# Performance work log

Measured on AMD Instinct MI355X. Metric: run time of the kernel, lower is better.

## Reference

```python
import jax, jax.numpy as jnp
import numpy as np

B, T, C, H = 2, 2048, 2048, 16
HD = C // H  # 128 head dim
ROPE_BASE = 10000.0


def setup_inputs() -> dict:
    key = jax.random.key(0)
    k0, k1, k2 = jax.random.split(key, 3)
    x = jax.random.normal(k0, (B, T, C), dtype=jnp.float32)
    W_attn = jax.random.normal(k1, (C, 3 * C), dtype=jnp.float32) * 0.02
    b_attn = jnp.zeros((3 * C,), dtype=jnp.float32)
    W_proj = jax.random.normal(k2, (C, C), dtype=jnp.float32) * 0.02
    b_proj = jnp.zeros((C,), dtype=jnp.float32)
    # freqs_cis = exp(i * t * theta_j), represented as (cos, sin), shape [T, HD//2]
    inv_freq = 1.0 / (ROPE_BASE ** (jnp.arange(0, HD, 2, dtype=jnp.float32) / HD))
    freqs = jnp.outer(jnp.arange(T, dtype=jnp.float32), inv_freq)
    return {"x": x, "W_attn": W_attn, "b_attn": b_attn, "W_proj": W_proj,
            "b_proj": b_proj, "cos": jnp.cos(freqs), "sin": jnp.sin(freqs)}


def _apply_rope(v, cos, sin):
    # v: [B, T, H, HD]; pairs (v[..., 2i], v[..., 2i+1]) rotated by angle freqs[t, i]
    vr = v.reshape(v.shape[:-1] + (-1, 2))
    x0, x1 = vr[..., 0], vr[..., 1]
    c = cos[None, :, None, :]  # [1, T, 1, HD//2]
    s = sin[None, :, None, :]
    o0 = x0 * c - x1 * s
    o1 = x0 * s + x1 * c
    return jnp.stack([o0, o1], axis=-1).reshape(v.shape)


def reference(x, W_attn, b_attn, W_proj, b_proj, cos, sin):
    Bv, Tv, Cv = x.shape
    qkv = x @ W_attn + b_attn                      # [B, T, 3C]
    q, k, v = jnp.split(qkv, 3, axis=-1)
    q = q.reshape(Bv, Tv, H, HD)
    k = k.reshape(Bv, Tv, H, HD)
    v = v.reshape(Bv, Tv, H, HD)
    q = _apply_rope(q, cos, sin)
    k = _apply_rope(k, cos, sin)
    scale = 1.0 / jnp.sqrt(jnp.float32(HD))
    att = jnp.einsum('bqhd,bkhd->bhqk', q, k) * scale
    causal = jnp.tril(jnp.ones((Tv, Tv), dtype=bool))
    att = jnp.where(causal[None, None], att, jnp.finfo(att.dtype).min)
    att = jax.nn.softmax(att, axis=-1)
    y = jnp.einsum('bhqk,bkhd->bqhd', att, v).reshape(Bv, Tv, Cv)
    return y @ W_proj + b_proj
```

## Files before the change

kernel.cpp:

```cpp
#include <hip/hip_runtime.h>

typedef unsigned short u16;
typedef __attribute__((ext_vector_type(8))) short short8;
typedef __attribute__((ext_vector_type(4))) float f32x4;

#define TSEQ 2048
#define NHEAD 16
#define HDIM 128

__device__ __forceinline__ u16 f2bf(float x) {
    unsigned u = __float_as_uint(x);
    return (u16)((u + 0x7fffu + ((u >> 16) & 1u)) >> 16);
}
__device__ __forceinline__ float b2f(u16 h) {
    return __uint_as_float(((unsigned)h) << 16);
}
__device__ __forceinline__ void async16(const void* g, void* l) {
    __builtin_amdgcn_global_load_lds((__attribute__((address_space(1))) void*)(void*)g,
                                     (__attribute__((address_space(3))) void*)l, 16, 0, 0);
}
__device__ __forceinline__ f32x4 zero4() {
    f32x4 z = {0.f, 0.f, 0.f, 0.f};
    return z;
}

template <int CTRL>
__device__ __forceinline__ float dppf(float x) {
    return __int_as_float(__builtin_amdgcn_mov_dpp(__float_as_int(x), CTRL, 0xf, 0xf, true));
}
__device__ __forceinline__ float dpp_max16(float x) {
    x = fmaxf(x, dppf<0xB1>(x));
    x = fmaxf(x, dppf<0x4E>(x));
    x = fmaxf(x, dppf<0x141>(x));
    x = fmaxf(x, dppf<0x140>(x));
    return x;
}
__device__ __forceinline__ float dpp_sum16(float x) {
    x += dppf<0xB1>(x);
    x += dppf<0x4E>(x);
    x += dppf<0x141>(x);
    x += dppf<0x140>(x);
    return x;
}

__global__ void cast_bf16(const float4* __restrict__ in, ushort4* __restrict__ out, int n4) {
    int i = blockIdx.x * 256 + threadIdx.x;
    if (i < n4) {
        float4 v = in[i];
        ushort4 o;
        o.x = f2bf(v.x); o.y = f2bf(v.y); o.z = f2bf(v.z); o.w = f2bf(v.w);
        out[i] = o;
    }
}

__global__ void transpose_cast(const float* __restrict__ in, u16* __restrict__ out, int K, int N) {
    __shared__ float tile[64][65];
    int n0 = blockIdx.x * 64, k0 = blockIdx.y * 64;
    int tx = threadIdx.x & 63, ty = threadIdx.x >> 6;
#pragma unroll
    for (int i = 0; i < 16; i++) {
        int r = ty + i * 4;
        tile[r][tx] = in[(size_t)(k0 + r) * N + n0 + tx];
    }
    __syncthreads();
#pragma unroll
    for (int i = 0; i < 16; i++) {
        int r = ty + i * 4;
        out[(size_t)(n0 + r) * K + k0 + tx] = f2bf(tile[tx][r]);
    }
}

template <int MODE>
__global__ __launch_bounds__(256) void gemm_bt(
    const u16* __restrict__ A, const u16* __restrict__ Bt, const float* __restrict__ bias,
    float* __restrict__ outf, u16* __restrict__ qb, u16* __restrict__ kb, u16* __restrict__ vT,
    const float* __restrict__ cosp, const float* __restrict__ sinp,
    int M, int N, int K) {
    __shared__ __align__(16) u16 smem[8704];
    u16* As = smem;
    u16* Bs = smem + 4096;
    const int tid = threadIdx.x;
    const int wave = tid >> 6, lane = tid & 63;
    const int low = lane & 15, quad = lane >> 4;
    const int m0 = blockIdx.y * 128, n0 = blockIdx.x * 128;
    const int wm = (wave >> 1) * 64, wn = (wave & 1) * 64;
    const int ldr = lane >> 2;
    const int ldc = (lane & 3) * 8;

    f32x4 acc[4][4];
#pragma unroll
    for (int i = 0; i < 4; i++)
#pragma unroll
        for (int j = 0; j < 4; j++) acc[i][j] = zero4();

    for (int k0 = 0; k0 < K; k0 += 32) {
#pragma unroll
        for (int c = 0; c < 2; ++c) {
            const int chunk = wave * 2 + c;
            const int row = chunk * 16 + ldr;
            async16(A + (size_t)(m0 + row) * K + k0 + ldc, As + chunk * 512);
            async16(Bt + (size_t)(n0 + row) * K + k0 + ldc, Bs + chunk * 512);
        }
        __syncthreads();
        short8 af[4], bfv[4];
#pragma unroll
        for (int i = 0; i < 4; i++) af[i] = *(const short8*)(As + (wm + i * 16 + low) * 32 + quad * 8);
#pragma unroll
        for (int j = 0; j < 4; j++) bfv[j] = *(const short8*)(Bs + (wn + j * 16 + low) * 32 + quad * 8);
#pragma unroll
        for (int i = 0; i < 4; i++)
#pragma unroll
            for (int j = 0; j < 4; j++)
                acc[i][j] = __builtin_amdgcn_mfma_f32_16x16x32_bf16(af[i], bfv[j], acc[i][j], 0, 0, 0);
        __syncthreads();
    }

    if (MODE == 1) {
#pragma unroll
        for (int j = 0; j < 4; j++) {
            const int ng = n0 + wn + j * 16 + low;
            const float bv = bias[ng];
#pragma unroll
            for (int i = 0; i < 4; i++) {
                const int rbase = m0 + wm + i * 16 + quad * 4;
#pragma unroll
                for (int r = 0; r < 4; r++)
                    outf[(size_t)(rbase + r) * N + ng] = acc[i][j][r] + bv;
            }
        }
        return;
    }

    const int which = n0 >> 11;
    const int h = (n0 & 2047) >> 7;
    const int b = m0 >> 11, t0 = m0 & 2047;
    float bv[4];
#pragma unroll
    for (int j = 0; j < 4; j++) bv[j] = bias[n0 + wn + j * 16 + low];
    u16* epi = smem;

    if (which < 2) {
        u16* dst = (which == 0 ? qb : kb) + (((size_t)(b * NHEAD + h)) * TSEQ + t0) * HDIM;
#pragma unroll
        for (int pass = 0; pass < 2; pass++) {
            if ((wave >> 1) == pass) {
#pragma unroll
                for (int i = 0; i < 4; i++)
#pragma unroll
                    for (int j = 0; j < 4; j++)
#pragma unroll
                        for (int r = 0; r < 4; r++)
                            epi[(i * 16 + quad * 4 + r) * 136 + wn + j * 16 + low] =
                                f2bf(acc[i][j][r] + bv[j]);
            }
            __syncthreads();
            const int row = tid >> 2, dp = (tid & 3) * 32;
            const int t = t0 + pass * 64 + row;
            u16 vals[32];
#pragma unroll
            for (int q = 0; q < 4; q++)
                *(short8*)(vals + q * 8) = *(const short8*)(epi + row * 136 + dp + q * 8);
            float cs4[16], sn4[16];
#pragma unroll
            for (int q = 0; q < 4; q++) {
                *(float4*)(cs4 + q * 4) = *(const float4*)(cosp + (size_t)t * 64 + (dp >> 1) + q * 4);
                *(float4*)(sn4 + q * 4) = *(const float4*)(sinp + (size_t)t * 64 + (dp >> 1) + q * 4);
            }
            u16 outv[32];
#pragma unroll
            for (int p = 0; p < 16; p++) {
                float x0 = b2f(vals[2 * p]), x1 = b2f(vals[2 * p + 1]);
                outv[2 * p] = f2bf(x0 * cs4[p] - x1 * sn4[p]);
                outv[2 * p + 1] = f2bf(x0 * sn4[p] + x1 * cs4[p]);
            }
            u16* dr = dst + (size_t)(pass * 64 + row) * HDIM + dp;
#pragma unroll
            for (int q = 0; q < 4; q++)
                *(short8*)(dr + q * 8) = *(const short8*)(outv + q * 8);
            __syncthreads();
        }
    } else {
        u16* dst = vT + ((size_t)(b * NHEAD + h)) * HDIM * TSEQ + t0;
#pragma unroll
        for (int pass = 0; pass < 2; pass++) {
            if ((wave & 1) == pass) {
#pragma unroll
                for (int i = 0; i < 4; i++)
#pragma unroll
                    for (int j = 0; j < 4; j++)
#pragma unroll
                        for (int r = 0; r < 4; r++)
                            epi[(j * 16 + low) * 136 + wm + i * 16 + quad * 4 + r] =
                                f2bf(acc[i][j][r] + bv[j]);
            }
            __syncthreads();
            const int drow = tid >> 2, tc = (tid & 3) * 32;
            u16* dr = dst + (size_t)(pass * 64 + drow) * TSEQ + tc;
#pragma unroll
            for (int q = 0; q < 4; q++)
                *(short8*)(dr + q * 8) = *(const short8*)(epi + drow * 136 + tc + q * 8);
            __syncthreads();
        }
    }
}


#define PH_PRE()                                           \
    {                                                      \
        __builtin_amdgcn_s_barrier();                      \
        asm volatile("s_waitcnt lgkmcnt(0)" ::: "memory"); \
        __builtin_amdgcn_sched_barrier(0);                 \
        __builtin_amdgcn_s_setprio(1);                     \
    }
#define PH_POST()                       \
    {                                   \
        __builtin_amdgcn_s_setprio(0);  \
        __builtin_amdgcn_s_barrier();   \
    }
#define PH_POSTV(N)                                            \
    {                                                          \
        __builtin_amdgcn_s_setprio(0);                         \
        asm volatile("s_waitcnt vmcnt(" #N ")" ::: "memory");  \
        __builtin_amdgcn_s_barrier();                          \
    }

#define STAGE(GP, GROW0, LB, KT)                                                                     \
    {                                                                                                \
        const int ktc__ = ((KT) < NT ? (KT) : NT - 1);                                               \
        const u16* g0__ = (GP) + (size_t)((GROW0) + wave * 16 + grow) * (size_t)K + ktc__ * 64 +     \
                          gslot * 8;                                                                 \
        u16* l0__ = (LB) + wave * 1024;                                                              \
        async16(g0__, l0__);                                                                         \
        async16(g0__ + (size_t)8 * K, l0__ + 512);                                                   \
    }

#define LDA4(BASE, MB)                                                              \
    {                                                                               \
        _Pragma("unroll") for (int mm = 0; mm < 4; ++mm) {                          \
            a[mm][0] = *(const short8*)((BASE) + aoff0 + ((MB) + mm) * 1024);       \
            a[mm][1] = *(const short8*)((BASE) + aoff1 + ((MB) + mm) * 1024);       \
        }                                                                           \
    }
#define LDB2(BASE, NB)                                                              \
    {                                                                               \
        _Pragma("unroll") for (int nn = 0; nn < 2; ++nn) {                          \
            b[(NB) + nn][0] = *(const short8*)((BASE) + boff0 + ((NB) + nn) * 1024);\
            b[(NB) + nn][1] = *(const short8*)((BASE) + boff1 + ((NB) + nn) * 1024);\
        }                                                                           \
    }
#define MFQ(MB, NB)                                                                                   \
    {                                                                                                 \
        _Pragma("unroll") for (int mm = 0; mm < 4; ++mm) _Pragma("unroll") for (int nn = 0; nn < 2;   \
                                                                                ++nn) {               \
            acc[(MB) + mm][(NB) + nn] = __builtin_amdgcn_mfma_f32_16x16x32_bf16(                      \
                a[mm][0], b[(NB) + nn][0], acc[(MB) + mm][(NB) + nn], 0, 0, 0);                       \
            acc[(MB) + mm][(NB) + nn] = __builtin_amdgcn_mfma_f32_16x16x32_bf16(                      \
                a[mm][1], b[(NB) + nn][1], acc[(MB) + mm][(NB) + nn], 0, 0, 0);                       \
        }                                                                                             \
    }

__global__ __launch_bounds__(512, 2) void gemm256(
    const u16* __restrict__ A, const u16* __restrict__ Bt, const float* __restrict__ bias,
    u16* __restrict__ qb, u16* __restrict__ kb, u16* __restrict__ vT,
    const float* __restrict__ cosp, const float* __restrict__ sinp,
    int M, int N, int K) {
    extern __shared__ u16 sm[];
    u16* const smA0 = sm;
    u16* const smB0 = sm + 16384;
    u16* const smA1 = sm + 32768;
    u16* const smB1 = sm + 49152;

    const int tid = threadIdx.x;
    const int wave = tid >> 6, lane = tid & 63;
    const int low = lane & 15, quad = lane >> 4;
    const int wr = wave >> 2, wc = wave & 3;
    const int m0 = blockIdx.y * 256, n0 = blockIdx.x * 256;
    const int NT = K >> 6;

    const int grow = lane >> 3;
    const int gslot = (lane & 7) ^ grow;

    const int swz = low & 7;
    const int arow = (wr * 128 + low) * 64;
    const int brow = (wc * 64 + low) * 64;
    const int aoff0 = arow + ((0 + quad) ^ swz) * 8;
    const int aoff1 = arow + ((4 + quad) ^ swz) * 8;
    const int boff0 = brow + ((0 + quad) ^ swz) * 8;
    const int boff1 = brow + ((4 + quad) ^ swz) * 8;

    f32x4 acc[8][4];
#pragma unroll
    for (int i = 0; i < 8; i++)
#pragma unroll
        for (int j = 0; j < 4; j++) acc[i][j] = zero4();
    short8 a[4][2], b[4][2];

    STAGE(A, m0, smA0, 0);
    STAGE(A, m0 + 128, smA0 + 8192, 0);
    STAGE(Bt, n0, smB0, 0);
    STAGE(Bt, n0 + 128, smB0 + 8192, 0);
    STAGE(A, m0, smA1, 1);
    STAGE(A, m0 + 128, smA1 + 8192, 1);
    asm volatile("s_waitcnt vmcnt(4)" ::: "memory");
    __builtin_amdgcn_s_barrier();

#pragma unroll 1
    for (int it = 0; it < (NT >> 1); ++it) {
        const int e = it * 2;
        LDA4(smA0, 0);
        LDB2(smB0, 0);
        STAGE(Bt, n0, smB1, e + 1);
        PH_PRE(); MFQ(0, 0); PH_POST();
        LDB2(smB0, 2);
        STAGE(Bt, n0 + 128, smB1 + 8192, e + 1);
        PH_PRE(); MFQ(0, 2); PH_POST();
        LDA4(smA0, 4);
        PH_PRE(); MFQ(4, 2); PH_POST();
        STAGE(A, m0, smA0, e + 2);
        PH_PRE(); MFQ(4, 0); PH_POSTV(2);
        LDA4(smA1, 0);
        LDB2(smB1, 0);
        STAGE(A, m0 + 128, smA0 + 8192, e + 2);
        PH_PRE(); MFQ(0, 0); PH_POST();
        LDB2(smB1, 2);
        STAGE(Bt, n0, smB0, e + 2);
        PH_PRE(); MFQ(0, 2); PH_POST();
        LDA4(smA1, 4);
        STAGE(Bt, n0 + 128, smB0 + 8192, e + 2);
        PH_PRE(); MFQ(4, 2); PH_POST();
        STAGE(A, m0, smA1, e + 3);
        STAGE(A, m0 + 128, smA1 + 8192, e + 3);
        PH_PRE(); MFQ(4, 0); PH_POSTV(4);
    }

    asm volatile("s_waitcnt vmcnt(0)" ::: "memory");
    __syncthreads();

    const int which = n0 >> 11;
    const int h0 = (n0 & 2047) >> 7;
    const int bb = m0 >> 11, t0 = m0 & 2047;
    float bvv[4];
#pragma unroll
    for (int nn = 0; nn < 4; ++nn) bvv[nn] = bias[n0 + wc * 64 + nn * 16 + low];

    if (which < 2) {
        u16* dstb = (which == 0 ? qb : kb);
        u16* epi = sm;
#pragma unroll
        for (int hh = 0; hh < 2; ++hh) {
            if ((wc >> 1) == hh) {
#pragma unroll
                for (int mm = 0; mm < 8; ++mm)
#pragma unroll
                    for (int nn = 0; nn < 4; ++nn)
#pragma unroll
                        for (int rr = 0; rr < 4; ++rr)
                            epi[(wr * 128 + mm * 16 + quad * 4 + rr) * 136 +
                                (wc & 1) * 64 + nn * 16 + low] = f2bf(acc[mm][nn][rr] + bvv[nn]);
            }
            __syncthreads();
            {
                const int row = tid >> 1, dh = (tid & 1) * 64;
                const int t = t0 + row;
                u16* dr = dstb + (((size_t)(bb * NHEAD + h0 + hh)) * TSEQ + t) * HDIM + dh;
                u16 vals[64];
#pragma unroll
                for (int qq = 0; qq < 8; ++qq)
                    *(short8*)(vals + qq * 8) = *(const short8*)(epi + row * 136 + dh + qq * 8);
                float csv[32], snv[32];
#pragma unroll
                for (int qq = 0; qq < 8; ++qq) {
                    *(float4*)(csv + qq * 4) =
                        *(const float4*)(cosp + (size_t)t * 64 + (dh >> 1) + qq * 4);
                    *(float4*)(snv + qq * 4) =
                        *(const float4*)(sinp + (size_t)t * 64 + (dh >> 1) + qq * 4);
                }
                u16 ov[64];
#pragma unroll
                for (int pp = 0; pp < 32; ++pp) {
                    float x0 = b2f(vals[2 * pp]), x1 = b2f(vals[2 * pp + 1]);
                    ov[2 * pp] = f2bf(x0 * csv[pp] - x1 * snv[pp]);
                    ov[2 * pp + 1] = f2bf(x0 * snv[pp] + x1 * csv[pp]);
                }
#pragma unroll
                for (int qq = 0; qq < 8; ++qq)
                    *(short8*)(dr + qq * 8) = *(const short8*)(ov + qq * 8);
            }
            __syncthreads();
        }
    } else {
        u16* epi = sm;
#pragma unroll
        for (int hh = 0; hh < 2; ++hh) {
            if ((wc >> 1) == hh) {
#pragma unroll
                for (int mm = 0; mm < 8; ++mm)
#pragma unroll
                    for (int nn = 0; nn < 4; ++nn)
#pragma unroll
                        for (int rr = 0; rr < 4; ++rr)
                            epi[((wc & 1) * 64 + nn * 16 + low) * 264 +
                                wr * 128 + mm * 16 + quad * 4 + rr] = f2bf(acc[mm][nn][rr] + bvv[nn]);
            }
            __syncthreads();
            {
                const int dd = tid >> 2, tc = (tid & 3) * 64;
                u16* dr = vT + ((size_t)(bb * NHEAD + h0 + hh) * HDIM + dd) * TSEQ + t0 + tc;
#pragma unroll
                for (int qq = 0; qq < 8; ++qq)
                    *(short8*)(dr + qq * 8) = *(const short8*)(epi + dd * 264 + tc + qq * 8);
            }
            __syncthreads();
        }
    }
}

__global__ __launch_bounds__(256) void flash_attn(const u16* __restrict__ qb, const u16* __restrict__ kb,
                                                  const u16* __restrict__ vT, u16* __restrict__ y) {
    __shared__ u16 Ks[64 * 128];
    __shared__ u16 Vs[128 * 64];
    __shared__ u16 Ps[4][16 * 72];
    const int tid = threadIdx.x;
    const int wave = tid >> 6, lane = tid & 63;
    const int low = lane & 15, quad = lane >> 4;
    const int bh = blockIdx.x;
    const int qt = 31 - blockIdx.y;
    const int q0 = qt * 64 + wave * 16;
    const float scale2 = 0.08838834764831845f * 1.44269504088896f;

    const u16* Qp = qb + ((size_t)bh * TSEQ + q0) * HDIM;
    short8 qf[4];
#pragma unroll
    for (int c = 0; c < 4; c++) qf[c] = *(const short8*)(Qp + (size_t)low * HDIM + c * 32 + quad * 8);

    f32x4 o[8];
#pragma unroll
    for (int d = 0; d < 8; d++) o[d] = zero4();
    float m_i[4], l_i[4];
#pragma unroll
    for (int r = 0; r < 4; r++) { m_i[r] = -1e30f; l_i[r] = 0.f; }

    const u16* Kb = kb + (size_t)bh * TSEQ * HDIM;
    const u16* Vb = vT + (size_t)bh * HDIM * TSEQ;
    u16* Pw = &Ps[wave][0];
    const int ntiles = qt + 1;

    const int krow = tid >> 4, kchunk = tid & 15;
    const int vrow = tid >> 3, vchunk = tid & 7;

    for (int kt = 0; kt < ntiles; ++kt) {
        const int kv0 = kt * 64;
#pragma unroll
        for (int j = 0; j < 4; j++) {
            const int row = j * 16 + krow;
            const int gc = kchunk ^ (row & 7);
            async16(Kb + (size_t)(kv0 + row) * HDIM + gc * 8, Ks + row * 128 + kchunk * 8);
        }
#pragma unroll
        for (int j = 0; j < 4; j++) {
            const int d = j * 32 + vrow;
            const int gc = vchunk ^ (d & 7);
            async16(Vb + (size_t)d * TSEQ + kv0 + gc * 8, Vs + d * 64 + vchunk * 8);
        }
        __syncthreads();

        f32x4 s[4];
#pragma unroll
        for (int h = 0; h < 4; h++) s[h] = zero4();
#pragma unroll
        for (int h = 0; h < 4; h++) {
            const int row = h * 16 + low;
#pragma unroll
            for (int c = 0; c < 4; c++) {
                const int cc = c * 4 + quad;
                short8 kf = *(const short8*)(Ks + row * 128 + (cc ^ (row & 7)) * 8);
                s[h] = __builtin_amdgcn_mfma_f32_16x16x32_bf16(qf[c], kf, s[h], 0, 0, 0);
            }
        }

        float alpha[4];
#pragma unroll
        for (int r = 0; r < 4; r++) {
            const int qg = q0 + quad * 4 + r;
            float sv[4];
#pragma unroll
            for (int h = 0; h < 4; h++)
                sv[h] = (kv0 + h * 16 + low <= qg) ? s[h][r] * scale2 : -1e30f;
            float mx = fmaxf(fmaxf(sv[0], sv[1]), fmaxf(sv[2], sv[3]));
            mx = dpp_max16(mx);
            float mnew = fmaxf(m_i[r], mx);
            alpha[r] = exp2f(m_i[r] - mnew);
            m_i[r] = mnew;
            float p0 = exp2f(sv[0] - mnew);
            float p1 = exp2f(sv[1] - mnew);
            float p2 = exp2f(sv[2] - mnew);
            float p3 = exp2f(sv[3] - mnew);
            float rs = (p0 + p1) + (p2 + p3);
            rs = dpp_sum16(rs);
            l_i[r] = l_i[r] * alpha[r] + rs;
            const int prow = (quad * 4 + r) * 72;
            Pw[prow + low] = f2bf(p0);
            Pw[prow + 16 + low] = f2bf(p1);
            Pw[prow + 32 + low] = f2bf(p2);
            Pw[prow + 48 + low] = f2bf(p3);
        }
        __threadfence_block();

#pragma unroll
        for (int d = 0; d < 8; ++d)
#pragma unroll
            for (int r = 0; r < 4; r++) o[d][r] *= alpha[r];

#pragma unroll
        for (int kc = 0; kc < 2; kc++) {
            short8 pf = *(const short8*)(Pw + low * 72 + kc * 32 + quad * 8);
#pragma unroll
            for (int dd = 0; dd < 8; ++dd) {
                const int vr = dd * 16 + low;
                const int cc = kc * 4 + quad;
                short8 vf = *(const short8*)(Vs + vr * 64 + (cc ^ (vr & 7)) * 8);
                o[dd] = __builtin_amdgcn_mfma_f32_16x16x32_bf16(pf, vf, o[dd], 0, 0, 0);
            }
        }
        __syncthreads();
    }

    const int b = bh >> 4, h = bh & 15;
#pragma unroll
    for (int r = 0; r < 4; r++) {
        float inv = 1.0f / l_i[r];
        size_t row = (size_t)(b * TSEQ + q0 + quad * 4 + r);
        u16* yp = y + row * 2048 + h * HDIM;
#pragma unroll
        for (int d = 0; d < 8; ++d) yp[d * 16 + low] = f2bf(o[d][r] * inv);
    }
}

extern "C" void kernel_launch(void* const* d_in, const int* in_sizes, int n_in,
                              void* d_out, int out_size, void* d_ws, size_t ws_size,
                              hipStream_t stream) {
    const float* x = (const float*)d_in[0];
    const float* Wa = (const float*)d_in[1];
    const float* ba = (const float*)d_in[2];
    const float* Wp = (const float*)d_in[3];
    const float* bp = (const float*)d_in[4];
    const float* cs = (const float*)d_in[5];
    const float* sn = (const float*)d_in[6];
    float* out = (float*)d_out;

    u16* xb = (u16*)d_ws;
    u16* Wab = xb + 8388608;
    u16* Wpb = Wab + 12582912;
    u16* qb = Wpb + 4194304;
    u16* kb = qb + 8388608;
    u16* vT = kb + 8388608;
    u16* y = xb;

    static bool attr_set = false;
    if (!attr_set) {
        hipFuncSetAttribute(reinterpret_cast<const void*>(gemm256),
                            hipFuncAttributeMaxDynamicSharedMemorySize, 131072);
        attr_set = true;
    }

    cast_bf16<<<8192, 256, 0, stream>>>((const float4*)x, (ushort4*)xb, 2097152);
    transpose_cast<<<dim3(96, 32), 256, 0, stream>>>(Wa, Wab, 2048, 6144);
    transpose_cast<<<dim3(32, 32), 256, 0, stream>>>(Wp, Wpb, 2048, 2048);
    gemm256<<<dim3(24, 16), 512, 131072, stream>>>(xb, Wab, ba, qb, kb, vT, cs, sn, 4096, 6144, 2048);
    flash_attn<<<dim3(32, 32), 256, 0, stream>>>(qb, kb, vT, y);
    gemm_bt<1><<<dim3(16, 32), 256, 0, stream>>>(y, Wpb, bp, out, nullptr, nullptr, nullptr, nullptr, nullptr, 4096, 2048, 2048);
}
```

Before: 423.4 us.

## Prefetch B tiles one stage earlier in QKV GEMM pipeline

```diff
diff --git a/kernel.cpp b/kernel.cpp
--- a/kernel.cpp
+++ b/kernel.cpp
@@ -130,78 +130,6 @@
         }
         return;
     }
-
-    const int which = n0 >> 11;
-    const int h = (n0 & 2047) >> 7;
-    const int b = m0 >> 11, t0 = m0 & 2047;
-    float bv[4];
-#pragma unroll
-    for (int j = 0; j < 4; j++) bv[j] = bias[n0 + wn + j * 16 + low];
-    u16* epi = smem;
-
-    if (which < 2) {
-        u16* dst = (which == 0 ? qb : kb) + (((size_t)(b * NHEAD + h)) * TSEQ + t0) * HDIM;
-#pragma unroll
-        for (int pass = 0; pass < 2; pass++) {
-            if ((wave >> 1) == pass) {
-#pragma unroll
-                for (int i = 0; i < 4; i++)
-#pragma unroll
-                    for (int j = 0; j < 4; j++)
-#pragma unroll
-                        for (int r = 0; r < 4; r++)
-                            epi[(i * 16 + quad * 4 + r) * 136 + wn + j * 16 + low] =
-                                f2bf(acc[i][j][r] + bv[j]);
-            }
-            __syncthreads();
-            const int row = tid >> 2, dp = (tid & 3) * 32;
-            const int t = t0 + pass * 64 + row;
-            u16 vals[32];
-#pragma unroll
-            for (int q = 0; q < 4; q++)
-                *(short8*)(vals + q * 8) = *(const short8*)(epi + row * 136 + dp + q * 8);
-            float cs4[16], sn4[16];
-#pragma unroll
-            for (int q = 0; q < 4; q++) {
-                *(float4*)(cs4 + q * 4) = *(const float4*)(cosp + (size_t)t * 64 + (dp >> 1) + q * 4);
-                *(float4*)(sn4 + q * 4) = *(const float4*)(sinp + (size_t)t * 64 + (dp >> 1) + q * 4);
-            }
-            u16 outv[32];
-#pragma unroll
-            for (int p = 0; p < 16; p++) {
-                float x0 = b2f(vals[2 * p]), x1 = b2f(vals[2 * p + 1]);
-                outv[2 * p] = f2bf(x0 * cs4[p] - x1 * sn4[p]);
-                outv[2 * p + 1] = f2bf(x0 * sn4[p] + x1 * cs4[p]);
-            }
-            u16* dr = dst + (size_t)(pass * 64 + row) * HDIM + dp;
-#pragma unroll
-            for (int q = 0; q < 4; q++)
-                *(short8*)(dr + q * 8) = *(const short8*)(outv + q * 8);
-            __syncthreads();
-        }
-    } else {
-        u16* dst = vT + ((size_t)(b * NHEAD + h)) * HDIM * TSEQ + t0;
-#pragma unroll
-        for (int pass = 0; pass < 2; pass++) {
-            if ((wave & 1) == pass) {
-#pragma unroll
-                for (int i = 0; i < 4; i++)
-#pragma unroll
-                    for (int j = 0; j < 4; j++)
-#pragma unroll
-                        for (int r = 0; r < 4; r++)
-                            epi[(j * 16 + low) * 136 + wm + i * 16 + quad * 4 + r] =
-                                f2bf(acc[i][j][r] + bv[j]);
-            }
-            __syncthreads();
-            const int drow = tid >> 2, tc = (tid & 3) * 32;
-            u16* dr = dst + (size_t)(pass * 64 + drow) * TSEQ + tc;
-#pragma unroll
-            for (int q = 0; q < 4; q++)
-                *(short8*)(dr + q * 8) = *(const short8*)(epi + drow * 136 + tc + q * 8);
-            __syncthreads();
-        }
-    }
 }
 
 
@@ -301,7 +229,9 @@
     STAGE(Bt, n0 + 128, smB0 + 8192, 0);
     STAGE(A, m0, smA1, 1);
     STAGE(A, m0 + 128, smA1 + 8192, 1);
-    asm volatile("s_waitcnt vmcnt(4)" ::: "memory");
+    STAGE(Bt, n0, smB1, 1);
+    STAGE(Bt, n0 + 128, smB1 + 8192, 1);
+    asm volatile("s_waitcnt vmcnt(8)" ::: "memory");
     __builtin_amdgcn_s_barrier();
 
 #pragma unroll 1
@@ -309,28 +239,28 @@
         const int e = it * 2;
         LDA4(smA0, 0);
         LDB2(smB0, 0);
-        STAGE(Bt, n0, smB1, e + 1);
         PH_PRE(); MFQ(0, 0); PH_POST();
         LDB2(smB0, 2);
-        STAGE(Bt, n0 + 128, smB1 + 8192, e + 1);
         PH_PRE(); MFQ(0, 2); PH_POST();
         LDA4(smA0, 4);
         PH_PRE(); MFQ(4, 2); PH_POST();
         STAGE(A, m0, smA0, e + 2);
-        PH_PRE(); MFQ(4, 0); PH_POSTV(2);
+        STAGE(Bt, n0, smB0, e + 2);
+        PH_PRE(); MFQ(4, 0); PH_POSTV(4);
         LDA4(smA1, 0);
         LDB2(smB1, 0);
         STAGE(A, m0 + 128, smA0 + 8192, e + 2);
+        STAGE(Bt, n0 + 128, smB0 + 8192, e + 2);
         PH_PRE(); MFQ(0, 0); PH_POST();
         LDB2(smB1, 2);
-        STAGE(Bt, n0, smB0, e + 2);
         PH_PRE(); MFQ(0, 2); PH_POST();
         LDA4(smA1, 4);
-        STAGE(Bt, n0 + 128, smB0 + 8192, e + 2);
         PH_PRE(); MFQ(4, 2); PH_POST();
         STAGE(A, m0, smA1, e + 3);
         STAGE(A, m0 + 128, smA1 + 8192, e + 3);
-        PH_PRE(); MFQ(4, 0); PH_POSTV(4);
+        STAGE(Bt, n0, smB1, e + 3);
+        STAGE(Bt, n0 + 128, smB1 + 8192, e + 3);
+        PH_PRE(); MFQ(4, 0); PH_POSTV(8);
     }
 
     asm volatile("s_waitcnt vmcnt(0)" ::: "memory");
```

After: 424.6 us. No clear change (+0.3%).
